# Optimization experiments

Hardware: AMD Instinct MI355X
Metric: run time of the kernel (lower is better)

## Reference

```python
import jax, jax.numpy as jnp
import numpy as np

B, S, D_MODEL, N_HEADS, D_K, D_V = 2, 2048, 1024, 16, 64, 64


def setup_inputs() -> dict:
    key = jax.random.key(0)
    ks = jax.random.split(key, 11)
    s_in = 1.0 / np.sqrt(D_MODEL)
    s_out = 1.0 / np.sqrt(N_HEADS * D_V)
    return {
        "Q": jax.random.normal(ks[0], (B, S, D_MODEL), jnp.float32),
        "K": jax.random.normal(ks[1], (B, S, D_MODEL), jnp.float32),
        "V": jax.random.normal(ks[2], (B, S, D_MODEL), jnp.float32),
        # per-head projection weights (stacked over heads), Linear-style: y = x @ W + b
        "Wq": jax.random.uniform(ks[3], (N_HEADS, D_MODEL, D_K), jnp.float32, -s_in, s_in),
        "bq": jax.random.uniform(ks[4], (N_HEADS, D_K), jnp.float32, -s_in, s_in),
        "Wk": jax.random.uniform(ks[5], (N_HEADS, D_MODEL, D_K), jnp.float32, -s_in, s_in),
        "bk": jax.random.uniform(ks[6], (N_HEADS, D_K), jnp.float32, -s_in, s_in),
        "Wv": jax.random.uniform(ks[7], (N_HEADS, D_MODEL, D_V), jnp.float32, -s_in, s_in),
        "bv": jax.random.uniform(ks[8], (N_HEADS, D_V), jnp.float32, -s_in, s_in),
        "Wo": jax.random.uniform(ks[9], (N_HEADS * D_V, D_MODEL), jnp.float32, -s_out, s_out),
        "bo": jax.random.uniform(ks[10], (D_MODEL,), jnp.float32, -s_out, s_out),
    }


def reference(Q, K, V, Wq, bq, Wk, bk, Wv, bv, Wo, bo):
    # Per-head projections, batched over heads: [B,H,S,dk/dv]
    QW = jnp.einsum("bsd,hdk->bhsk", Q, Wq) + bq[None, :, None, :]
    KW = jnp.einsum("bsd,hdk->bhsk", K, Wk) + bk[None, :, None, :]
    VW = jnp.einsum("bsd,hdv->bhsv", V, Wv) + bv[None, :, None, :]
    scores = jnp.einsum("bhsk,bhtk->bhst", QW, KW)  # [B,H,S,S]
    # Faithful to torch source: softmax(scores)/d_k**1/2 == softmax(scores)/(2*d_k)
    attn = jax.nn.softmax(scores, axis=-1) * (1.0 / (2.0 * D_K))
    heads = jnp.einsum("bhst,bhtv->bhsv", attn, VW)  # [B,H,S,dv]
    # concat heads along feature dim -> [B,S,H*dv], then output projection
    concat = heads.transpose(0, 2, 1, 3).reshape(B, S, N_HEADS * D_V)
    return concat @ Wo + bo
```

## Files before the change

kernel.cpp:

```cpp
#include <hip/hip_runtime.h>

#define BB 2
#define SS 2048
#define DM 1024
#define HH 16
#define DK 64
#define LOG2E 1.44269504088896340736f

typedef __attribute__((ext_vector_type(8))) short short8;
typedef __attribute__((ext_vector_type(4))) float f32x4;
typedef __attribute__((ext_vector_type(16))) float f32x16;

#define MFMA16(a, b, c) __builtin_amdgcn_mfma_f32_16x16x32_bf16(a, b, c, 0, 0, 0)
#define MFMA32(a, b, c) __builtin_amdgcn_mfma_f32_32x32x16_bf16(a, b, c, 0, 0, 0)

#if __has_builtin(__builtin_amdgcn_exp2f)
#define EXP2(x) __builtin_amdgcn_exp2f(x)
#else
#define EXP2(x) __expf((x) * 0.6931471805599453f)
#endif

#define WAITV(N) asm volatile("s_waitcnt vmcnt(" #N ")" ::: "memory")
#define BAR() __builtin_amdgcn_s_barrier()

#define FRAG(buf, row, col) \
    (*(const short8*)&buf[(row) * 64 + ((col) ^ (((row) & 7) << 3))])
#define FRAGV(buf, row, col) \
    (*(const short8*)&buf[(row) * 128 + (((((col) >> 3) ^ ((row) & 15))) << 3)])

static __device__ __forceinline__ unsigned short f2bf(float f) {
    unsigned u = __builtin_bit_cast(unsigned, f);
    u += 0x7fffu + ((u >> 16) & 1u);
    return (unsigned short)(u >> 16);
}

static __device__ __forceinline__ void gld16(const void* g, void* l) {
    __builtin_amdgcn_global_load_lds(
        (const __attribute__((address_space(1))) unsigned int*)g,
        (__attribute__((address_space(3))) unsigned int*)l, 16, 0, 0);
}

__global__ __launch_bounds__(256) void cvt3_kernel(
    const float* __restrict__ p0, const float* __restrict__ p1,
    const float* __restrict__ p2, unsigned short* __restrict__ o0,
    unsigned short* __restrict__ o1, unsigned short* __restrict__ o2) {
    const int m = blockIdx.y;
    const float* in = m == 0 ? p0 : (m == 1 ? p1 : p2);
    unsigned short* out = m == 0 ? o0 : (m == 1 ? o1 : o2);
    const int i = (blockIdx.x * 256 + threadIdx.x) * 8;
    float4 a = *(const float4*)(in + i);
    float4 b = *(const float4*)(in + i + 4);
    union { unsigned short u[8]; uint4 v; } x;
    x.u[0] = f2bf(a.x); x.u[1] = f2bf(a.y); x.u[2] = f2bf(a.z); x.u[3] = f2bf(a.w);
    x.u[4] = f2bf(b.x); x.u[5] = f2bf(b.y); x.u[6] = f2bf(b.z); x.u[7] = f2bf(b.w);
    *(uint4*)(out + i) = x.v;
}

__global__ __launch_bounds__(256) void wtrans4_kernel(
    const float* __restrict__ Wq, const float* __restrict__ Wk,
    const float* __restrict__ Wv, const float* __restrict__ Wo,
    unsigned short* __restrict__ Wqt, unsigned short* __restrict__ Wkt,
    unsigned short* __restrict__ Wvt, unsigned short* __restrict__ Wot) {
    __shared__ float t[64][65];
    const int which = blockIdx.y;
    const float* in;
    unsigned short* out;
    int r0, c0, C;
    if (which < 3) {
        in = which == 0 ? Wq : (which == 1 ? Wk : Wv);
        out = which == 0 ? Wqt : (which == 1 ? Wkt : Wvt);
        const int h = blockIdx.x >> 4;
        r0 = (blockIdx.x & 15) * 64; c0 = 0; C = DK;
        in += (size_t)h * DM * DK;
        out += (size_t)h * DK * DM;
    } else {
        in = Wo; out = Wot;
        r0 = (blockIdx.x & 15) * 64; c0 = (blockIdx.x >> 4) * 64; C = DM;
    }
    const int lr = threadIdx.x & 63, gg = threadIdx.x >> 6;
    #pragma unroll
    for (int p = 0; p < 16; ++p) {
        const int r = p * 4 + gg;
        t[r][lr] = in[(size_t)(r0 + r) * C + c0 + lr];
    }
    __syncthreads();
    #pragma unroll
    for (int p = 0; p < 16; ++p) {
        const int c = p * 4 + gg;
        out[(size_t)(c0 + c) * DM + r0 + lr] = f2bf(t[lr][c]);
    }
}

#define GSTAGE(Ap, Btp, k0, pp)                                              \
    do {                                                                     \
        _Pragma("unroll")                                                    \
        for (int i = 0; i < 4; ++i) {                                        \
            const int idx = tid + i * 256;                                   \
            const int row = idx >> 3;                                        \
            const int cs = ((idx & 7) ^ (row & 7)) * 8;                      \
            gld16(&Ap[(size_t)(r0 + row) * DM + (k0) + cs], &As[pp][idx * 8]); \
            gld16(&Btp[(size_t)(n0 + row) * DM + (k0) + cs], &Bs[pp][idx * 8]); \
        }                                                                    \
    } while (0)

#define GCOMPUTE(pp)                                                         \
    do {                                                                     \
        _Pragma("unroll")                                                    \
        for (int kc = 0; kc < 2; ++kc) {                                     \
            short8 a[4], b[4];                                               \
            _Pragma("unroll")                                                \
            for (int i = 0; i < 4; ++i) {                                    \
                a[i] = FRAG(As[pp], wr + i * 16 + lr, kc * 32 + lg * 8);     \
                b[i] = FRAG(Bs[pp], wc + i * 16 + lr, kc * 32 + lg * 8);     \
            }                                                                \
            __builtin_amdgcn_s_setprio(1);                                   \
            _Pragma("unroll")                                                \
            for (int mi = 0; mi < 4; ++mi)                                   \
                _Pragma("unroll")                                            \
                for (int ni = 0; ni < 4; ++ni)                               \
                    acc[mi][ni] = MFMA16(a[mi], b[ni], acc[mi][ni]);         \
            __builtin_amdgcn_s_setprio(0);                                   \
        }                                                                    \
    } while (0)

#define GEMM_MAIN(Ap, Btp)                                                   \
    GSTAGE(Ap, Btp, 0, 0);                                                   \
    for (int k = 0; k < 14 * 64; k += 128) {                                 \
        GSTAGE(Ap, Btp, k + 64, 1);                                          \
        WAITV(8); BAR();                                                     \
        GCOMPUTE(0);                                                         \
        BAR();                                                               \
        GSTAGE(Ap, Btp, k + 128, 0);                                         \
        WAITV(8); BAR();                                                     \
        GCOMPUTE(1);                                                         \
        BAR();                                                               \
    }                                                                        \
    GSTAGE(Ap, Btp, 15 * 64, 1);                                             \
    WAITV(8); BAR();                                                         \
    GCOMPUTE(0);                                                             \
    BAR();                                                                   \
    WAITV(0); BAR();                                                         \
    GCOMPUTE(1);

__global__ __launch_bounds__(256) void qkv_gemm_kernel(
    const unsigned short* __restrict__ Qb, const unsigned short* __restrict__ Kb,
    const unsigned short* __restrict__ Vb,
    const unsigned short* __restrict__ Wqt, const unsigned short* __restrict__ Wkt,
    const unsigned short* __restrict__ Wvt,
    const float* __restrict__ bq, const float* __restrict__ bk,
    const float* __restrict__ bv,
    unsigned short* __restrict__ QWp, unsigned short* __restrict__ KWp,
    unsigned short* __restrict__ VWt) {
    __shared__ unsigned short As[2][128 * 64];
    __shared__ unsigned short Bs[2][128 * 64];
    const int z = blockIdx.z;
    const unsigned short* A  = z == 0 ? Qb : (z == 1 ? Kb : Vb);
    const unsigned short* Bt = z == 0 ? Wqt : (z == 1 ? Wkt : Wvt);
    const float* bias = z == 0 ? bq : (z == 1 ? bk : bv);
    const int tid = threadIdx.x;
    const int r0 = blockIdx.x * 128, n0 = blockIdx.y * 128;
    const int w = tid >> 6, lane = tid & 63, lr = lane & 15, lg = lane >> 4;
    const int wr = (w >> 1) * 64, wc = (w & 1) * 64;

    const f32x4 zf = {0.f, 0.f, 0.f, 0.f};
    f32x4 acc[4][4];
    #pragma unroll
    for (int mi = 0; mi < 4; ++mi)
        #pragma unroll
        for (int ni = 0; ni < 4; ++ni) acc[mi][ni] = zf;

    GEMM_MAIN(A, Bt);

    const float scale = (z == 0) ? LOG2E : 1.0f;
    #pragma unroll
    for (int ni = 0; ni < 4; ++ni) {
        const int col = n0 + wc + ni * 16 + lr;
        const float bb = bias[col];
        #pragma unroll
        for (int mi = 0; mi < 4; ++mi) {
            const int rbase = r0 + wr + mi * 16 + lg * 4;
            const f32x4 v = acc[mi][ni];
            if (z == 2) {
                const int b = rbase >> 11, s = rbase & (SS - 1);
                const int h = col >> 6, vv = col & 63;
                union { unsigned short u[4]; unsigned long long q; } x;
                #pragma unroll
                for (int j = 0; j < 4; ++j) x.u[j] = f2bf(v[j] + bb);
                *(unsigned long long*)&VWt[((size_t)(b * HH + h) * 64 + vv) * SS + s] = x.q;
            } else {
                unsigned short* C = z == 0 ? QWp : KWp;
                #pragma unroll
                for (int j = 0; j < 4; ++j)
                    C[(size_t)(rbase + j) * DM + col] = f2bf((v[j] + bb) * scale);
            }
        }
    }
}

__global__ __launch_bounds__(256) void outproj_kernel(
    const unsigned short* __restrict__ A, const unsigned short* __restrict__ Bt,
    const float* __restrict__ bias, float* __restrict__ Cout) {
    __shared__ unsigned short As[2][128 * 64];
    __shared__ unsigned short Bs[2][128 * 64];
    const int tid = threadIdx.x;
    const int r0 = blockIdx.x * 128, n0 = blockIdx.y * 128;
    const int w = tid >> 6, lane = tid & 63, lr = lane & 15, lg = lane >> 4;
    const int wr = (w >> 1) * 64, wc = (w & 1) * 64;

    const f32x4 zf = {0.f, 0.f, 0.f, 0.f};
    f32x4 acc[4][4];
    #pragma unroll
    for (int mi = 0; mi < 4; ++mi)
        #pragma unroll
        for (int ni = 0; ni < 4; ++ni) acc[mi][ni] = zf;

    GEMM_MAIN(A, Bt);

    #pragma unroll
    for (int ni = 0; ni < 4; ++ni) {
        const int col = n0 + wc + ni * 16 + lr;
        const float bb = bias[col];
        #pragma unroll
        for (int mi = 0; mi < 4; ++mi) {
            const int rbase = r0 + wr + mi * 16 + lg * 4;
            const f32x4 v = acc[mi][ni];
            #pragma unroll
            for (int j = 0; j < 4; ++j)
                Cout[(size_t)(rbase + j) * DM + col] = v[j] + bb;
        }
    }
}

__global__ __launch_bounds__(256, 2) void attn_kernel(
    const unsigned short* __restrict__ QW,
    const unsigned short* __restrict__ KW,
    const unsigned short* __restrict__ VWt,
    unsigned short* __restrict__ CC) {
    __shared__ unsigned short Ks[2][128 * 64];
    __shared__ unsigned short Vs[2][64 * 128];
    const int tid = threadIdx.x;
    const int w = tid >> 6, lane = tid & 63;
    const int ql = lane & 31, hi = lane >> 5, hi8 = hi * 8;

    const int wgid = blockIdx.x;
    const int kk = wgid >> 3;
    const int bh = (kk >> 4) * 8 + (wgid & 7);
    const int b = bh >> 4, h = bh & 15;
    const int row0 = (kk & 15) * 128;
    const int q = row0 + w * 32 + ql;

    short8 qf[4];
    const unsigned short* Qp = QW + ((size_t)b * SS + q) * DM + h * DK;
    #pragma unroll
    for (int kc = 0; kc < 4; ++kc)
        qf[kc] = *(const short8*)(Qp + kc * 16 + hi8);

    const unsigned short* Kp = KW + (size_t)b * SS * DM + h * DK;
    const unsigned short* Vt = VWt + (size_t)bh * 64 * SS;

#define STAGE(t0, pp)                                                        \
    do {                                                                     \
        _Pragma("unroll")                                                    \
        for (int i = 0; i < 4; ++i) {                                        \
            const int idx = tid + i * 256;                                   \
            const int kr = idx >> 3;                                         \
            const int kc8 = ((idx & 7) ^ (kr & 7)) * 8;                      \
            gld16(&Kp[(size_t)((t0) + kr) * DM + kc8], &Ks[pp][idx * 8]);    \
            const int vr = idx >> 4;                                         \
            const int vc8 = ((idx & 15) ^ (vr & 15)) * 8;                    \
            gld16(&Vt[(size_t)vr * SS + (t0) + vc8], &Vs[pp][idx * 8]);      \
        }                                                                    \
    } while (0)

    const f32x16 z16 = {0.f};
    const short8 ones = {(short)0x3F80, (short)0x3F80, (short)0x3F80, (short)0x3F80,
                         (short)0x3F80, (short)0x3F80, (short)0x3F80, (short)0x3F80};
    f32x16 o0 = z16, o1 = z16, lv = z16;

#define PACK2(sx, pa0, pa1)                                                      \
    do {                                                                         \
        unsigned x, x2, y, y2, u, u2, v, v2;                                     \
        asm("v_cvt_pk_bf16_f32 %0, %1, %2" : "=v"(x)  : "v"(sx[0]), "v"(sx[1])); \
        asm("v_cvt_pk_bf16_f32 %0, %1, %2" : "=v"(x2) : "v"(sx[2]), "v"(sx[3])); \
        asm("v_cvt_pk_bf16_f32 %0, %1, %2" : "=v"(y)  : "v"(sx[4]), "v"(sx[5])); \
        asm("v_cvt_pk_bf16_f32 %0, %1, %2" : "=v"(y2) : "v"(sx[6]), "v"(sx[7])); \
        asm("v_cvt_pk_bf16_f32 %0, %1, %2" : "=v"(u)  : "v"(sx[8]), "v"(sx[9])); \
        asm("v_cvt_pk_bf16_f32 %0, %1, %2" : "=v"(u2) : "v"(sx[10]), "v"(sx[11])); \
        asm("v_cvt_pk_bf16_f32 %0, %1, %2" : "=v"(v)  : "v"(sx[12]), "v"(sx[13])); \
        asm("v_cvt_pk_bf16_f32 %0, %1, %2" : "=v"(v2) : "v"(sx[14]), "v"(sx[15])); \
        asm("v_permlane32_swap_b32 %0, %1" : "+v"(x),  "+v"(y));                 \
        asm("v_permlane32_swap_b32 %0, %1" : "+v"(x2), "+v"(y2));                \
        asm("v_permlane32_swap_b32 %0, %1" : "+v"(u),  "+v"(v));                 \
        asm("v_permlane32_swap_b32 %0, %1" : "+v"(u2), "+v"(v2));                \
        union { unsigned uu[4]; short8 s8; } k0, k1;                             \
        k0.uu[0] = x; k0.uu[1] = x2; k0.uu[2] = y; k0.uu[3] = y2;                \
        k1.uu[0] = u; k1.uu[1] = u2; k1.uu[2] = v; k1.uu[3] = v2;                \
        pa0 = k0.s8; pa1 = k1.s8;                                                \
    } while (0)

#define PVC(pp, sx, c)                                                           \
    do {                                                                         \
        _Pragma("unroll")                                                        \
        for (int r = 0; r < 16; ++r) sx[r] = EXP2(sx[r]);                        \
        short8 pa0, pa1;                                                         \
        PACK2(sx, pa0, pa1);                                                     \
        __builtin_amdgcn_s_setprio(1);                                           \
        o0 = MFMA32(FRAGV(Vs[pp], ql, (c) * 32 + hi8), pa0, o0);                 \
        lv = MFMA32(ones, pa0, lv);                                              \
        o1 = MFMA32(FRAGV(Vs[pp], 32 + ql, (c) * 32 + hi8), pa0, o1);            \
        o0 = MFMA32(FRAGV(Vs[pp], ql, (c) * 32 + 16 + hi8), pa1, o0);            \
        lv = MFMA32(ones, pa1, lv);                                              \
        o1 = MFMA32(FRAGV(Vs[pp], 32 + ql, (c) * 32 + 16 + hi8), pa1, o1);       \
        __builtin_amdgcn_s_setprio(0);                                           \
    } while (0)

#define COMPUTE(pp)                                                              \
    do {                                                                         \
        f32x16 s0, s1, s2, s3;                                                   \
        __builtin_amdgcn_s_setprio(1);                                           \
        s0 = MFMA32(FRAG(Ks[pp], ql, hi8), qf[0], z16);                          \
        s1 = MFMA32(FRAG(Ks[pp], 32 + ql, hi8), qf[0], z16);                     \
        s2 = MFMA32(FRAG(Ks[pp], 64 + ql, hi8), qf[0], z16);                     \
        s3 = MFMA32(FRAG(Ks[pp], 96 + ql, hi8), qf[0], z16);                     \
        _Pragma("unroll")                                                        \
        for (int kc = 1; kc < 4; ++kc) {                                         \
            s0 = MFMA32(FRAG(Ks[pp], ql, kc * 16 + hi8), qf[kc], s0);            \
            s1 = MFMA32(FRAG(Ks[pp], 32 + ql, kc * 16 + hi8), qf[kc], s1);       \
            s2 = MFMA32(FRAG(Ks[pp], 64 + ql, kc * 16 + hi8), qf[kc], s2);       \
            s3 = MFMA32(FRAG(Ks[pp], 96 + ql, kc * 16 + hi8), qf[kc], s3);       \
        }                                                                        \
        __builtin_amdgcn_s_setprio(0);                                           \
        PVC(pp, s0, 0);                                                          \
        PVC(pp, s1, 1);                                                          \
        PVC(pp, s2, 2);                                                          \
        PVC(pp, s3, 3);                                                          \
    } while (0)

    STAGE(0, 0);
    for (int t = 0; t < 14; t += 2) {
        STAGE((t + 1) * 128, 1);
        WAITV(8); BAR();
        COMPUTE(0);
        BAR();
        STAGE((t + 2) * 128, 0);
        WAITV(8); BAR();
        COMPUTE(1);
        BAR();
    }
    STAGE(15 * 128, 1);
    WAITV(8); BAR();
    COMPUTE(0);
    BAR();
    WAITV(0); BAR();
    COMPUTE(1);
#undef STAGE
#undef COMPUTE
#undef PVC

    const float inv = 1.0f / (lv[0] * 128.0f);
    unsigned short* cp = CC + ((size_t)b * SS + q) * DM + h * DK;
    #pragma unroll
    for (int vt = 0; vt < 2; ++vt) {
        const f32x16 ov = vt ? o1 : o0;
        #pragma unroll
        for (int m2 = 0; m2 < 4; ++m2) {
            union { unsigned short u[4]; unsigned long long q8; } pk;
            #pragma unroll
            for (int c = 0; c < 4; ++c) pk.u[c] = f2bf(ov[m2 * 4 + c] * inv);
            *(unsigned long long*)(cp + vt * 32 + m2 * 8 + hi * 4) = pk.q8;
        }
    }
}

extern "C" void kernel_launch(void* const* d_in, const int* in_sizes, int n_in,
                              void* d_out, int out_size, void* d_ws, size_t ws_size,
                              hipStream_t stream) {
    const float* Q  = (const float*)d_in[0];
    const float* K  = (const float*)d_in[1];
    const float* V  = (const float*)d_in[2];
    const float* Wq = (const float*)d_in[3];
    const float* bq = (const float*)d_in[4];
    const float* Wk = (const float*)d_in[5];
    const float* bk = (const float*)d_in[6];
    const float* Wv = (const float*)d_in[7];
    const float* bv = (const float*)d_in[8];
    const float* Wo = (const float*)d_in[9];
    const float* bo = (const float*)d_in[10];
    float* out = (float*)d_out;

    unsigned short* ws = (unsigned short*)d_ws;
    const size_t MK = (size_t)BB * SS * DM;
    const size_t WK = (size_t)DM * DM;
    unsigned short* Qb  = ws;
    unsigned short* Kb  = Qb + MK;
    unsigned short* Vb  = Kb + MK;
    unsigned short* Wqt = Vb + MK;
    unsigned short* Wkt = Wqt + WK;
    unsigned short* Wvt = Wkt + WK;
    unsigned short* Wot = Wvt + WK;
    unsigned short* QWp = Wot + WK;
    unsigned short* KWp = QWp + MK;
    unsigned short* VWt = KWp + MK;
    unsigned short* CCp = Qb;

    dim3 blk(256);
    const int M = BB * SS;

    hipLaunchKernelGGL(cvt3_kernel, dim3(MK / 2048, 3), blk, 0, stream,
                       Q, K, V, Qb, Kb, Vb);

    hipLaunchKernelGGL(wtrans4_kernel, dim3(256, 4), blk, 0, stream,
                       Wq, Wk, Wv, Wo, Wqt, Wkt, Wvt, Wot);

    hipLaunchKernelGGL(qkv_gemm_kernel, dim3(M / 128, 8, 3), blk, 0, stream,
                       Qb, Kb, Vb, Wqt, Wkt, Wvt, bq, bk, bv, QWp, KWp, VWt);

    hipLaunchKernelGGL(attn_kernel, dim3(512), blk, 0, stream,
                       QWp, KWp, VWt, CCp);

    hipLaunchKernelGGL(outproj_kernel, dim3(M / 128, 8), blk, 0, stream,
                       CCp, Wot, bo, out);
}
```

Baseline: 119.5 us.

## Merge conversion kernels into one launch and halve output-projection tile width

Merges the activation bf16 conversion and the weight transpose kernels into a single prep kernel, which removes one launch and lets the two phases overlap. The output projection now uses 128x64 tiles with its own double-buffered staging loop, doubling the block count from 256 to 512 so the device's compute units are better filled. The cost is less operand reuse per block and more total A-tile reloads.

```diff
diff --git a/kernel.cpp b/kernel.cpp
--- a/kernel.cpp
+++ b/kernel.cpp
@@ -40,42 +40,47 @@
         (__attribute__((address_space(3))) unsigned int*)l, 16, 0, 0);
 }
 
-__global__ __launch_bounds__(256) void cvt3_kernel(
-    const float* __restrict__ p0, const float* __restrict__ p1,
-    const float* __restrict__ p2, unsigned short* __restrict__ o0,
-    unsigned short* __restrict__ o1, unsigned short* __restrict__ o2) {
-    const int m = blockIdx.y;
-    const float* in = m == 0 ? p0 : (m == 1 ? p1 : p2);
-    unsigned short* out = m == 0 ? o0 : (m == 1 ? o1 : o2);
-    const int i = (blockIdx.x * 256 + threadIdx.x) * 8;
-    float4 a = *(const float4*)(in + i);
-    float4 b = *(const float4*)(in + i + 4);
-    union { unsigned short u[8]; uint4 v; } x;
-    x.u[0] = f2bf(a.x); x.u[1] = f2bf(a.y); x.u[2] = f2bf(a.z); x.u[3] = f2bf(a.w);
-    x.u[4] = f2bf(b.x); x.u[5] = f2bf(b.y); x.u[6] = f2bf(b.z); x.u[7] = f2bf(b.w);
-    *(uint4*)(out + i) = x.v;
-}
-
-__global__ __launch_bounds__(256) void wtrans4_kernel(
+__global__ __launch_bounds__(256) void prep_kernel(
+    const float* __restrict__ Q, const float* __restrict__ K,
+    const float* __restrict__ V,
     const float* __restrict__ Wq, const float* __restrict__ Wk,
     const float* __restrict__ Wv, const float* __restrict__ Wo,
+    unsigned short* __restrict__ Qb, unsigned short* __restrict__ Kb,
+    unsigned short* __restrict__ Vb,
     unsigned short* __restrict__ Wqt, unsigned short* __restrict__ Wkt,
     unsigned short* __restrict__ Wvt, unsigned short* __restrict__ Wot) {
     __shared__ float t[64][65];
-    const int which = blockIdx.y;
+    const int bid = blockIdx.x;
+    if (bid < 6144) {
+        const int m = bid >> 11;
+        const int bx = bid & 2047;
+        const float* in = m == 0 ? Q : (m == 1 ? K : V);
+        unsigned short* out = m == 0 ? Qb : (m == 1 ? Kb : Vb);
+        const int i = (bx * 256 + threadIdx.x) * 8;
+        float4 a = *(const float4*)(in + i);
+        float4 b = *(const float4*)(in + i + 4);
+        union { unsigned short u[8]; uint4 v; } x;
+        x.u[0] = f2bf(a.x); x.u[1] = f2bf(a.y); x.u[2] = f2bf(a.z); x.u[3] = f2bf(a.w);
+        x.u[4] = f2bf(b.x); x.u[5] = f2bf(b.y); x.u[6] = f2bf(b.z); x.u[7] = f2bf(b.w);
+        *(uint4*)(out + i) = x.v;
+        return;
+    }
+    const int idx = bid - 6144;
+    const int which = idx >> 8;
+    const int bx = idx & 255;
     const float* in;
     unsigned short* out;
     int r0, c0, C;
     if (which < 3) {
         in = which == 0 ? Wq : (which == 1 ? Wk : Wv);
         out = which == 0 ? Wqt : (which == 1 ? Wkt : Wvt);
-        const int h = blockIdx.x >> 4;
-        r0 = (blockIdx.x & 15) * 64; c0 = 0; C = DK;
+        const int h = bx >> 4;
+        r0 = (bx & 15) * 64; c0 = 0; C = DK;
         in += (size_t)h * DM * DK;
         out += (size_t)h * DK * DM;
     } else {
         in = Wo; out = Wot;
-        r0 = (blockIdx.x & 15) * 64; c0 = (blockIdx.x >> 4) * 64; C = DM;
+        r0 = (bx & 15) * 64; c0 = (bx >> 4) * 64; C = DM;
     }
     const int lr = threadIdx.x & 63, gg = threadIdx.x >> 6;
     #pragma unroll
@@ -201,23 +206,80 @@
     const unsigned short* __restrict__ A, const unsigned short* __restrict__ Bt,
     const float* __restrict__ bias, float* __restrict__ Cout) {
     __shared__ unsigned short As[2][128 * 64];
-    __shared__ unsigned short Bs[2][128 * 64];
+    __shared__ unsigned short Bs[2][64 * 64];
     const int tid = threadIdx.x;
-    const int r0 = blockIdx.x * 128, n0 = blockIdx.y * 128;
+    const int r0 = blockIdx.x * 128, n0 = blockIdx.y * 64;
     const int w = tid >> 6, lane = tid & 63, lr = lane & 15, lg = lane >> 4;
-    const int wr = (w >> 1) * 64, wc = (w & 1) * 64;
+    const int wr = (w >> 1) * 64, wc = (w & 1) * 32;
 
     const f32x4 zf = {0.f, 0.f, 0.f, 0.f};
-    f32x4 acc[4][4];
+    f32x4 acc[4][2];
     #pragma unroll
     for (int mi = 0; mi < 4; ++mi)
         #pragma unroll
-        for (int ni = 0; ni < 4; ++ni) acc[mi][ni] = zf;
-
-    GEMM_MAIN(A, Bt);
-
-    #pragma unroll
-    for (int ni = 0; ni < 4; ++ni) {
+        for (int ni = 0; ni < 2; ++ni) acc[mi][ni] = zf;
+
+#define OSTAGE(k0, pp)                                                       \
+    do {                                                                     \
+        _Pragma("unroll")                                                    \
+        for (int i = 0; i < 4; ++i) {                                        \
+            const int idx = tid + i * 256;                                   \
+            const int row = idx >> 3;                                        \
+            const int cs = ((idx & 7) ^ (row & 7)) * 8;                      \
+            gld16(&A[(size_t)(r0 + row) * DM + (k0) + cs], &As[pp][idx * 8]); \
+        }                                                                    \
+        _Pragma("unroll")                                                    \
+        for (int i = 0; i < 2; ++i) {                                        \
+            const int idx = tid + i * 256;                                   \
+            const int row = idx >> 3;                                        \
+            const int cs = ((idx & 7) ^ (row & 7)) * 8;                      \
+            gld16(&Bt[(size_t)(n0 + row) * DM + (k0) + cs], &Bs[pp][idx * 8]); \
+        }                                                                    \
+    } while (0)
+
+#define OCOMP(pp)                                                            \
+    do {                                                                     \
+        _Pragma("unroll")                                                    \
+        for (int kc = 0; kc < 2; ++kc) {                                     \
+            short8 a[4], b[2];                                               \
+            _Pragma("unroll")                                                \
+            for (int i = 0; i < 4; ++i)                                      \
+                a[i] = FRAG(As[pp], wr + i * 16 + lr, kc * 32 + lg * 8);     \
+            _Pragma("unroll")                                                \
+            for (int i = 0; i < 2; ++i)                                      \
+                b[i] = FRAG(Bs[pp], wc + i * 16 + lr, kc * 32 + lg * 8);     \
+            __builtin_amdgcn_s_setprio(1);                                   \
+            _Pragma("unroll")                                                \
+            for (int mi = 0; mi < 4; ++mi)                                   \
+                _Pragma("unroll")                                            \
+                for (int ni = 0; ni < 2; ++ni)                               \
+                    acc[mi][ni] = MFMA16(a[mi], b[ni], acc[mi][ni]);         \
+            __builtin_amdgcn_s_setprio(0);                                   \
+        }                                                                    \
+    } while (0)
+
+    OSTAGE(0, 0);
+    for (int k = 0; k < 14 * 64; k += 128) {
+        OSTAGE(k + 64, 1);
+        WAITV(6); BAR();
+        OCOMP(0);
+        BAR();
+        OSTAGE(k + 128, 0);
+        WAITV(6); BAR();
+        OCOMP(1);
+        BAR();
+    }
+    OSTAGE(15 * 64, 1);
+    WAITV(6); BAR();
+    OCOMP(0);
+    BAR();
+    WAITV(0); BAR();
+    OCOMP(1);
+#undef OSTAGE
+#undef OCOMP
+
+    #pragma unroll
+    for (int ni = 0; ni < 2; ++ni) {
         const int col = n0 + wc + ni * 16 + lr;
         const float bb = bias[col];
         #pragma unroll
@@ -406,11 +468,9 @@
     dim3 blk(256);
     const int M = BB * SS;
 
-    hipLaunchKernelGGL(cvt3_kernel, dim3(MK / 2048, 3), blk, 0, stream,
-                       Q, K, V, Qb, Kb, Vb);
-
-    hipLaunchKernelGGL(wtrans4_kernel, dim3(256, 4), blk, 0, stream,
-                       Wq, Wk, Wv, Wo, Wqt, Wkt, Wvt, Wot);
+    hipLaunchKernelGGL(prep_kernel, dim3(7168), blk, 0, stream,
+                       Q, K, V, Wq, Wk, Wv, Wo,
+                       Qb, Kb, Vb, Wqt, Wkt, Wvt, Wot);
 
     hipLaunchKernelGGL(qkv_gemm_kernel, dim3(M / 128, 8, 3), blk, 0, stream,
                        Qb, Kb, Vb, Wqt, Wkt, Wvt, bq, bk, bv, QWp, KWp, VWt);
@@ -418,6 +478,6 @@
     hipLaunchKernelGGL(attn_kernel, dim3(512), blk, 0, stream,
                        QWp, KWp, VWt, CCp);
 
-    hipLaunchKernelGGL(outproj_kernel, dim3(M / 128, 8), blk, 0, stream,
+    hipLaunchKernelGGL(outproj_kernel, dim3(M / 128, DM / 64), blk, 0, stream,
                        CCp, Wot, bo, out);
 }
```

After: 117.5 us. No clear change (-1.7%).
